# Kernel optimization log

Measured on AMD Instinct MI355X. Metric: run time of the kernel, lower is better.

Reference implementation:

```python
import jax, jax.numpy as jnp
import numpy as np

N = 100000      # total nodes (100 graphs x 1000 nodes each)
G = 100         # graphs per batch
F_IN = 12       # node_features (temporal window)
F_OUT = 32      # DCRNN hidden size (hardcoded in module)
K = 5           # diffusion (Chebyshev) steps (hardcoded)
C = 4           # num_classes
E = 16 * N      # edges: ring (N) + random (15N)


def setup_inputs() -> dict:
    key = jax.random.key(0)
    ks = jax.random.split(key, 12)
    x = jax.random.normal(ks[0], (N, F_IN), dtype=jnp.float32)
    ring = jnp.arange(N, dtype=jnp.int32)
    src = jnp.concatenate([ring, jax.random.randint(ks[1], (15 * N,), 0, N, dtype=jnp.int32)])
    dst = jnp.concatenate([(ring + 1) % N, jax.random.randint(ks[2], (15 * N,), 0, N, dtype=jnp.int32)])
    edge_index = jnp.stack([src, dst])  # [2, E]
    edge_weight = jax.random.uniform(ks[3], (E,), dtype=jnp.float32, minval=0.1, maxval=1.0)
    batch = (jnp.arange(N, dtype=jnp.int32) * G) // N  # sorted graph ids, 1000 nodes per graph
    s = 0.1
    return dict(
        x=x, edge_index=edge_index, edge_weight=edge_weight, batch=batch,
        W_z=jax.random.normal(ks[4], (2, K, F_IN + F_OUT, F_OUT), jnp.float32) * s,
        b_z=jax.random.normal(ks[5], (F_OUT,), jnp.float32) * s,
        W_r=jax.random.normal(ks[6], (2, K, F_IN + F_OUT, F_OUT), jnp.float32) * s,
        b_r=jax.random.normal(ks[7], (F_OUT,), jnp.float32) * s,
        W_h=jax.random.normal(ks[8], (2, K, F_IN + F_OUT, F_OUT), jnp.float32) * s,
        b_h=jax.random.normal(ks[9], (F_OUT,), jnp.float32) * s,
        W_lin=jax.random.normal(ks[10], (F_OUT, C), jnp.float32) * s,
        b_lin=jax.random.normal(ks[11], (C,), jnp.float32) * s,
    )


def reference(x, edge_index, edge_weight, batch, W_z, b_z, W_r, b_r, W_h, b_h, W_lin, b_lin):
    row, col = edge_index[0], edge_index[1]
    # weighted in/out degrees (to_dense_adj sums duplicate edges, same as segment_sum)
    deg_out_inv = 1.0 / jax.ops.segment_sum(edge_weight, row, num_segments=N)
    deg_in_inv = 1.0 / jax.ops.segment_sum(edge_weight, col, num_segments=N)
    norm_out = deg_out_inv[row][:, None]  # per-edge 1/deg_out(src)
    norm_in = deg_in_inv[row][:, None]    # per-edge 1/deg_in(src), as in DConv

    def prop_fwd(h):  # out[dst] += h[src]/deg_out[src]
        return jax.ops.segment_sum(norm_out * h[row], col, num_segments=N)

    def prop_rev(h):  # reverse (transposed) diffusion: out[src] += h[dst]/deg_in[src]
        return jax.ops.segment_sum(norm_in * h[col], row, num_segments=N)

    def dconv(Xc, W, b):
        # Chebyshev diffusion conv, W: [2, K, F_in+F_out, F_out]
        H = Xc @ (W[0, 0] + W[1, 0])
        T1o, T1i = prop_fwd(Xc), prop_rev(Xc)
        H = H + T1o @ W[0, 1] + T1i @ W[1, 1]
        T0o = T0i = Xc
        for k in range(2, K):
            T2o = 2.0 * prop_fwd(T1o) - T0o
            T2i = 2.0 * prop_rev(T1i) - T0i
            H = H + T2o @ W[0, k] + T2i @ W[1, k]
            T0o, T1o = T1o, T2o
            T0i, T1i = T1i, T2i
        return H + b

    # GRU gating with zero-initialized hidden state (H=None in module)
    Hst = jnp.zeros((N, F_OUT), x.dtype)
    XH = jnp.concatenate([x, Hst], axis=1)
    Z = jax.nn.sigmoid(dconv(XH, W_z, b_z))
    R = jax.nn.sigmoid(dconv(XH, W_r, b_r))
    XRH = jnp.concatenate([x, R * Hst], axis=1)
    H_tilde = jnp.tanh(dconv(XRH, W_h, b_h))
    H = Z * Hst + (1.0 - Z) * H_tilde

    h = jax.nn.relu(H) @ W_lin + b_lin            # [N, C]
    sums = jax.ops.segment_sum(h, batch, num_segments=G)
    counts = jax.ops.segment_sum(jnp.ones((N,), h.dtype), batch, num_segments=G)
    return sums / counts[:, None]                 # global_mean_pool -> [G, C]
```

## Files before the change

### kernel.cpp

```cpp
#include <hip/hip_runtime.h>
#include <math.h>

#define NN    100000
#define GG    100
#define FIN   12
#define FOUT  32
#define KD    5
#define CC    4
#define EE    1600000
#define ROWS  108
#define NBF   782
#define NBINS 1564
#define NBC   512
#define CHUNK 3125
#define TOTR  (2 * CHUNK)
#define NSEG  (NBINS * NBC)
#define SUBMAX 3072

__device__ __forceinline__ unsigned bfr(float f) {
    unsigned u = __float_as_uint(f);
    return (u + 0x7FFFu + ((u >> 16) & 1u)) >> 16;
}
__device__ __forceinline__ unsigned pack2(float a, float b) {
    return bfr(a) | (bfr(b) << 16);
}
#define BLO(u) __uint_as_float((u) << 16)
#define BHI(u) __uint_as_float((u) & 0xFFFF0000u)

__device__ __forceinline__ int chunk_of_block(int b) {
    return ((b & 7) << 6) | (b >> 3);
}


__global__ __launch_bounds__(512) void k_hist(const int* __restrict__ ei,
                                              int* __restrict__ hist_g) {
    __shared__ int hist[NBINS];
    for (int i = threadIdx.x; i < NBINS; i += 512) hist[i] = 0;
    __syncthreads();
    int chunk = chunk_of_block(blockIdx.x);
    int lo = chunk * CHUNK, hi = lo + CHUNK;
    for (int e = lo + threadIdx.x; e < hi; e += 512) {
        int s = ei[e], d = ei[EE + e];
        atomicAdd(&hist[d >> 7], 1);
        atomicAdd(&hist[NBF + (s >> 7)], 1);
    }
    __syncthreads();
    for (int i = threadIdx.x; i < NBINS; i += 512)
        hist_g[i * NBC + chunk] = hist[i];
}

__global__ __launch_bounds__(1024) void k_scan1(
        int* __restrict__ g, int* __restrict__ bsum,
        const float* __restrict__ Wz_in, const float* __restrict__ Wh_in,
        float* __restrict__ Wz, float* __restrict__ Wh,
        const float* __restrict__ b_lin, float* __restrict__ out,
        const float* __restrict__ x, uint2* __restrict__ xb) {
    __shared__ int sh[1024];
    int t = threadIdx.x;
    int i = blockIdx.x * 1024 + t;
    int v = g[i];
    sh[t] = v;
    __syncthreads();
    for (int d = 1; d < 1024; d <<= 1) {
        int x2 = sh[t];
        if (t >= d) x2 += sh[t - d];
        __syncthreads();
        sh[t] = x2;
        __syncthreads();
    }
    g[i] = sh[t] - v;
    if (t == 1023) bsum[blockIdx.x] = sh[1023];

    if (i < 2 * ROWS * FOUT) {
        int sel = i / (ROWS * FOUT);
        int rem = i - sel * ROWS * FOUT;
        int r = rem / FOUT;
        int f = rem - r * FOUT;
        int b = r / 12;
        int ii = r - b * 12;
        const float* Ws = sel ? Wh_in : Wz_in;
        float vv;
        if (b == 0)
            vv = Ws[(0 * KD + 0) * 44 * 32 + ii * 32 + f] + Ws[(1 * KD + 0) * 44 * 32 + ii * 32 + f];
        else if (b <= 4)
            vv = Ws[(0 * KD + b) * 44 * 32 + ii * 32 + f];
        else
            vv = Ws[(1 * KD + (b - 4)) * 44 * 32 + ii * 32 + f];
        (sel ? Wh : Wz)[r * FOUT + f] = vv;
    }
    int u = i - 2 * ROWS * FOUT;
    if (u >= 0 && u < GG * CC) out[u] = b_lin[u & 3];
    if (i < 3 * NN) {
        int n = i / 3, c = i - n * 3;
        float4 vf = *(const float4*)(x + (size_t)n * FIN + c * 4);
        xb[(size_t)n * 3 + c] = make_uint2(pack2(vf.x, vf.y), pack2(vf.z, vf.w));
    }
}

__global__ __launch_bounds__(1024) void k_scan3(int* __restrict__ g,
                                                const int* __restrict__ bsum,
                                                int* __restrict__ off,
                                                int* __restrict__ off_node) {
    __shared__ int sh[1024];
    int t = threadIdx.x;
    sh[t] = (t < blockIdx.x) ? bsum[t] : 0;
    __syncthreads();
    for (int d = 512; d > 0; d >>= 1) {
        if (t < d) sh[t] += sh[t + d];
        __syncthreads();
    }
    int base = sh[0];
    int i = blockIdx.x * 1024 + t;
    int v = g[i] + base;
    g[i] = v;
    if ((i & (NBC - 1)) == 0) off[i / NBC] = v;
    if (i == 0) { off[NBINS] = 2 * EE; off_node[2 * NN] = 2 * EE; }
}

__global__ __launch_bounds__(512) void k_place(const int* __restrict__ ei,
                                               const float* __restrict__ ew,
                                               const int* __restrict__ base_g,
                                               int2* __restrict__ recA) {
    __shared__ int2 ldsrec[TOTR];
    __shared__ int  lofs[NBINS];
    __shared__ int  cur[NBINS];
    __shared__ int  sbase[NBINS];
    __shared__ unsigned short binof[TOTR];
    int* psum = (int*)binof;
    int t = threadIdx.x;
    int chunk = chunk_of_block(blockIdx.x);

    for (int bin = t; bin < NBINS; bin += 512) {
        int b0 = base_g[bin * NBC + chunk];
        int b1;
        if (chunk < NBC - 1)      b1 = base_g[bin * NBC + chunk + 1];
        else if (bin < NBINS - 1) b1 = base_g[(bin + 1) * NBC];
        else                      b1 = 2 * EE;
        sbase[bin] = b0;
        lofs[bin] = b1 - b0;
        cur[bin] = 0;
    }
    __syncthreads();

    int i0 = t * 4;
    int v0 = 0, v1 = 0, v2 = 0, v3 = 0;
    if (i0 + 0 < NBINS) v0 = lofs[i0];
    if (i0 + 1 < NBINS) v1 = lofs[i0 + 1];
    if (i0 + 2 < NBINS) v2 = lofs[i0 + 2];
    if (i0 + 3 < NBINS) v3 = lofs[i0 + 3];
    int s = v0 + v1 + v2 + v3;
    psum[t] = s;
    __syncthreads();
    for (int d = 1; d < 512; d <<= 1) {
        int x = psum[t];
        if (t >= d) x += psum[t - d];
        __syncthreads();
        psum[t] = x;
        __syncthreads();
    }
    int run = psum[t] - s;
    __syncthreads();
    if (i0 + 0 < NBINS) { lofs[i0]     = run; run += v0; }
    if (i0 + 1 < NBINS) { lofs[i0 + 1] = run; run += v1; }
    if (i0 + 2 < NBINS) { lofs[i0 + 2] = run; run += v2; }
    if (i0 + 3 < NBINS) { lofs[i0 + 3] = run; run += v3; }
    __syncthreads();

    int lo = chunk * CHUNK;
    for (int e = lo + t; e < lo + CHUNK; e += 512) {
        int s2 = ei[e], d2 = ei[EE + e];
        float w = ew[e];
        int bf = d2 >> 7;
        int pf = lofs[bf] + atomicAdd(&cur[bf], 1);
        ldsrec[pf] = make_int2(s2 | ((d2 & 127) << 17), __float_as_int(w));
        binof[pf] = (unsigned short)bf;
        int br = NBF + (s2 >> 7);
        int pr = lofs[br] + atomicAdd(&cur[br], 1);
        ldsrec[pr] = make_int2(d2 | ((s2 & 127) << 17), __float_as_int(w));
        binof[pr] = (unsigned short)br;
    }
    __syncthreads();

    for (int i = t; i < TOTR; i += 512) {
        int b = binof[i];
        recA[sbase[b] + (i - lofs[b])] = ldsrec[i];
    }
}

__global__ __launch_bounds__(256) void k_subcsr(
        const int* __restrict__ off, const int2* __restrict__ recA,
        const float* __restrict__ x,
        int* __restrict__ off_node, int* __restrict__ rec2,
        float* __restrict__ dinv_in, float* __restrict__ dinv_out,
        uint2* __restrict__ gA) {
    __shared__ int2  seg[SUBMAX];
    __shared__ int   hist[128];
    __shared__ int   lofs[128];
    __shared__ int   cur[128];
    __shared__ float wsum[128];
    __shared__ float dl[128];
    int b = blockIdx.x;
    int t = threadIdx.x;
    if (t < 128) { hist[t] = 0; wsum[t] = 0.f; }
    __syncthreads();
    int e0 = off[b], e1 = off[b + 1];
    int cnt = e1 - e0;
    bool stg = (cnt <= SUBMAX);
    if (stg) {
        for (int i = t; i < cnt; i += 256) {
            int2 r = recA[e0 + i];
            seg[i] = r;
            int loc = r.x >> 17;
            atomicAdd(&hist[loc], 1);
            atomicAdd(&wsum[loc], __int_as_float(r.y));
        }
    } else {
        for (int i = t; i < cnt; i += 256) {
            int2 r = recA[e0 + i];
            int loc = r.x >> 17;
            atomicAdd(&hist[loc], 1);
            atomicAdd(&wsum[loc], __int_as_float(r.y));
        }
    }
    __syncthreads();
    if (t < 128) lofs[t] = hist[t];
    __syncthreads();
    for (int d = 1; d < 128; d <<= 1) {
        int v = 0;
        if (t < 128 && t >= d) v = lofs[t - d];
        __syncthreads();
        if (t < 128) lofs[t] += v;
        __syncthreads();
    }
    bool rev = b >= NBF;
    int base = (rev ? b - NBF : b) * 128;
    if (t < 128) {
        int ex = lofs[t] - hist[t];
        lofs[t] = ex;
        cur[t] = 0;
        int node = base + t;
        if (node < NN) {
            off_node[(rev ? NN : 0) + node] = e0 + ex;
            float inv = 1.f / wsum[t];
            dl[t] = inv;
            if (rev) dinv_out[node] = inv;
            else     dinv_in[node]  = inv;
        }
    }
    __syncthreads();
    if (stg) {
        for (int i = t; i < cnt; i += 256) {
            int rx = seg[i].x;
            int loc = rx >> 17;
            int pos = e0 + lofs[loc] + atomicAdd(&cur[loc], 1);
            rec2[pos] = rx & 0x1FFFF;
        }
    } else {
        for (int i = t; i < cnt; i += 256) {
            int rx = recA[e0 + i].x;
            int loc = rx >> 17;
            int pos = e0 + lofs[loc] + atomicAdd(&cur[loc], 1);
            rec2[pos] = rx & 0x1FFFF;
        }
    }
    if (rev) {
        __syncthreads();
        for (int i = t; i < 128 * 3; i += 256) {
            int loc = i / 3, cc = i - loc * 3;
            int node = base + loc;
            if (node < NN) {
                float4 v = *(const float4*)(x + (size_t)node * FIN + cc * 4);
                float sc = dl[loc];
                gA[(size_t)node * 3 + cc] =
                    make_uint2(pack2(v.x * sc, v.y * sc), pack2(v.z * sc, v.w * sc));
            }
        }
    }
}

#define LREC 2048
__global__ __launch_bounds__(256) void k_gather(
        const int* __restrict__ off_node, const int* __restrict__ rec2,
        const uint2* __restrict__ gIn, const uint2* __restrict__ hIn,
        const uint2* __restrict__ prevF, const uint2* __restrict__ prevR,
        const float* __restrict__ dinv_in, const float* __restrict__ dinv_out,
        uint2* __restrict__ outF, uint2* __restrict__ outR,
        uint2* __restrict__ gOut, float c) {
    __shared__ int lrec[LREC];
    int xcd = blockIdx.x & 7;
    int grp = blockIdx.x >> 3;
    bool rev = xcd >= 4;
    int dbase = rev ? NN : 0;
    int ub = (grp * 4 + (xcd & 3)) * 256;
    int lin = ub + threadIdx.x;

    int u1 = ub + 255; if (u1 > 3 * NN - 1) u1 = 3 * NN - 1;
    int node0 = ub / 3, node1 = u1 / 3;
    int w0 = off_node[dbase + node0];
    int w1 = off_node[dbase + node1 + 1];
    int wn = w1 - w0;
    bool useLds = (wn <= LREC);
    if (useLds) {
        for (int i = threadIdx.x; i < wn; i += 256) lrec[i] = rec2[w0 + i];
    }
    __syncthreads();

    if (lin < 3 * NN) {
        int node = lin / 3;
        int ch = lin - node * 3;
        int i0 = dbase + node;
        int e0 = off_node[i0], e1 = off_node[i0 + 1];
        const uint2* in = rev ? hIn : gIn;

        float ax = 0.f, ay = 0.f, az = 0.f, aw = 0.f;
        float bx = 0.f, by = 0.f, bz = 0.f, bw = 0.f;
        if (useLds) {
            int a0 = e0 - w0, a1 = e1 - w0;
            int e = a0;
            for (; e + 7 < a1; e += 8) {
                int n0 = lrec[e],     n1 = lrec[e + 1], n2 = lrec[e + 2], n3 = lrec[e + 3];
                int n4 = lrec[e + 4], n5 = lrec[e + 5], n6 = lrec[e + 6], n7 = lrec[e + 7];
                uint2 v0 = in[(size_t)n0 * 3 + ch];
                uint2 v1 = in[(size_t)n1 * 3 + ch];
                uint2 v2 = in[(size_t)n2 * 3 + ch];
                uint2 v3 = in[(size_t)n3 * 3 + ch];
                uint2 v4 = in[(size_t)n4 * 3 + ch];
                uint2 v5 = in[(size_t)n5 * 3 + ch];
                uint2 v6 = in[(size_t)n6 * 3 + ch];
                uint2 v7 = in[(size_t)n7 * 3 + ch];
                ax += BLO(v0.x); ay += BHI(v0.x); az += BLO(v0.y); aw += BHI(v0.y);
                bx += BLO(v1.x); by += BHI(v1.x); bz += BLO(v1.y); bw += BHI(v1.y);
                ax += BLO(v2.x); ay += BHI(v2.x); az += BLO(v2.y); aw += BHI(v2.y);
                bx += BLO(v3.x); by += BHI(v3.x); bz += BLO(v3.y); bw += BHI(v3.y);
                ax += BLO(v4.x); ay += BHI(v4.x); az += BLO(v4.y); aw += BHI(v4.y);
                bx += BLO(v5.x); by += BHI(v5.x); bz += BLO(v5.y); bw += BHI(v5.y);
                ax += BLO(v6.x); ay += BHI(v6.x); az += BLO(v6.y); aw += BHI(v6.y);
                bx += BLO(v7.x); by += BHI(v7.x); bz += BLO(v7.y); bw += BHI(v7.y);
            }
            for (; e < a1; ++e) {
                int n0 = lrec[e];
                uint2 v0 = in[(size_t)n0 * 3 + ch];
                ax += BLO(v0.x); ay += BHI(v0.x); az += BLO(v0.y); aw += BHI(v0.y);
            }
        } else {
            for (int e = e0; e < e1; ++e) {
                int n0 = rec2[e];
                uint2 v0 = in[(size_t)n0 * 3 + ch];
                ax += BLO(v0.x); ay += BHI(v0.x); az += BLO(v0.y); aw += BHI(v0.y);
            }
        }
        ax += bx; ay += by; az += bz; aw += bw;

        float sc = rev ? c * dinv_in[node] : c;
        ax *= sc; ay *= sc; az *= sc; aw *= sc;

        size_t o = (size_t)node * 3 + ch;
        if (prevF) {
            uint2 p = (rev ? prevR : prevF)[o];
            ax -= BLO(p.x); ay -= BHI(p.x); az -= BLO(p.y); aw -= BHI(p.y);
        }
        (rev ? outR : outF)[o] = make_uint2(pack2(ax, ay), pack2(az, aw));
        if (!rev && gOut) {
            float g = dinv_out[node];
            gOut[o] = make_uint2(pack2(g * ax, g * ay), pack2(g * az, g * aw));
        }
    }
}


__global__ __launch_bounds__(256) void k_fused(
        const float* __restrict__ x, const uint2* __restrict__ TS2,
        const float* __restrict__ Wz, const float* __restrict__ Wh,
        const float* __restrict__ bz, const float* __restrict__ bh,
        const float* __restrict__ Wlin, float* __restrict__ out) {
    __shared__ float rows[128][13];
    __shared__ float red[256 * CC];
    int g = blockIdx.x >> 3;
    int seg = blockIdx.x & 7;
    int base = g * 1000 + seg * 125;
    int tid = threadIdx.x;
    int lane = tid & 63;
    int wave = tid >> 6;
    int f0 = __builtin_amdgcn_readfirstlane(wave * 8);

    float az0[8], ah0[8], az1[8], ah1[8];
#pragma unroll
    for (int fi = 0; fi < 8; ++fi) {
        float vz = bz[f0 + fi], vh = bh[f0 + fi];
        az0[fi] = vz; ah0[fi] = vh; az1[fi] = vz; ah1[fi] = vh;
    }
    bool act1 = (lane + 64) < 125;

    for (int b = 0; b < 9; ++b) {
        __syncthreads();
        if (b == 0) {
            const float* src = x + (size_t)base * FIN;
            for (int q = tid; q < 375; q += 256) {
                float4 v = *(const float4*)(src + q * 4);
                int e = q * 4;
                int n0 = e / 12,       i0 = e - n0 * 12;       rows[n0][i0] = v.x;
                int n1 = (e + 1) / 12, i1 = (e + 1) - n1 * 12; rows[n1][i1] = v.y;
                int n2 = (e + 2) / 12, i2 = (e + 2) - n2 * 12; rows[n2][i2] = v.z;
                int n3 = (e + 3) / 12, i3 = (e + 3) - n3 * 12; rows[n3][i3] = v.w;
            }
        } else {
            const uint2* Tb = TS2 + (size_t)(b - 1) * NN * 3;
            for (int q = tid; q < 375; q += 256) {
                int n = q / 3, cc = q - n * 3;
                uint2 v = Tb[(size_t)(base + n) * 3 + cc];
                rows[n][cc * 4 + 0] = BLO(v.x);
                rows[n][cc * 4 + 1] = BHI(v.x);
                rows[n][cc * 4 + 2] = BLO(v.y);
                rows[n][cc * 4 + 3] = BHI(v.y);
            }
        }
        __syncthreads();
        const float* wzr = Wz + b * 12 * FOUT + f0;
        const float* whr = Wh + b * 12 * FOUT + f0;
#pragma unroll
        for (int i = 0; i < FIN; ++i) {
            float v0 = rows[lane][i];
            float v1 = rows[lane + 64][i];
#pragma unroll
            for (int fi = 0; fi < 8; ++fi) {
                float wz = wzr[i * FOUT + fi];
                float wh = whr[i * FOUT + fi];
                az0[fi] = fmaf(v0, wz, az0[fi]);
                az1[fi] = fmaf(v1, wz, az1[fi]);
                ah0[fi] = fmaf(v0, wh, ah0[fi]);
                ah1[fi] = fmaf(v1, wh, ah1[fi]);
            }
        }
    }

    float o[CC] = {0.f, 0.f, 0.f, 0.f};
#pragma unroll
    for (int fi = 0; fi < 8; ++fi) {
        float z = 1.f / (1.f + __expf(-az0[fi]));
        float e2 = __expf(2.f * ah0[fi]);
        float th = 1.f - 2.f / (e2 + 1.f);
        float hv = fmaxf((1.f - z) * th, 0.f);
#pragma unroll
        for (int c = 0; c < CC; ++c) o[c] = fmaf(hv, Wlin[(f0 + fi) * 4 + c], o[c]);
    }
    if (act1) {
#pragma unroll
        for (int fi = 0; fi < 8; ++fi) {
            float z = 1.f / (1.f + __expf(-az1[fi]));
            float e2 = __expf(2.f * ah1[fi]);
            float th = 1.f - 2.f / (e2 + 1.f);
            float hv = fmaxf((1.f - z) * th, 0.f);
#pragma unroll
            for (int c = 0; c < CC; ++c) o[c] = fmaf(hv, Wlin[(f0 + fi) * 4 + c], o[c]);
        }
    }

#pragma unroll
    for (int c = 0; c < CC; ++c) red[tid * CC + c] = o[c];
    __syncthreads();
    for (int st = 128; st > 0; st >>= 1) {
        if (tid < st) {
#pragma unroll
            for (int c = 0; c < CC; ++c) red[tid * CC + c] += red[(tid + st) * CC + c];
        }
        __syncthreads();
    }
    if (tid == 0) {
#pragma unroll
        for (int c = 0; c < CC; ++c) atomicAdd(out + g * CC + c, red[c] * 0.001f);
    }
}


extern "C" void kernel_launch(void* const* d_in, const int* in_sizes, int n_in,
                              void* d_out, int out_size, void* d_ws, size_t ws_size,
                              hipStream_t stream) {
    const float* x     = (const float*)d_in[0];
    const int*   ei    = (const int*)d_in[1];
    const float* ew    = (const float*)d_in[2];
    const float* W_z   = (const float*)d_in[4];
    const float* b_z   = (const float*)d_in[5];
    const float* W_h   = (const float*)d_in[8];
    const float* b_h   = (const float*)d_in[9];
    const float* W_lin = (const float*)d_in[10];
    const float* b_lin = (const float*)d_in[11];
    float* out = (float*)d_out;

    int*   rec2     = (int*)d_ws;
    unsigned* TSb   = (unsigned*)(rec2 + 2 * (size_t)EE);
    int2*  recA     = (int2*)TSb;
    int*   hist_g   = rec2;
    int*   bsumS    = rec2 + NSEG;
    unsigned* gAu   = TSb + (size_t)8 * NN * 6 + 1600000;
    unsigned* gBu   = gAu + (size_t)NN * 6;
    unsigned* xbu   = gBu + (size_t)NN * 6;
    float* dinv_in  = (float*)(xbu + (size_t)NN * 6);
    float* dinv_out = dinv_in + NN;
    float* Wz       = dinv_out + NN;
    float* Wh       = Wz + ROWS * FOUT;
    int*   off      = (int*)(Wh + ROWS * FOUT);
    int*   off_node = off + NBINS + 1;

    uint2* TS2 = (uint2*)TSb;
    uint2* T1o = TS2 + (size_t)0 * NN * 3;
    uint2* T2o = TS2 + (size_t)1 * NN * 3;
    uint2* T3o = TS2 + (size_t)2 * NN * 3;
    uint2* T4o = TS2 + (size_t)3 * NN * 3;
    uint2* T1i = TS2 + (size_t)4 * NN * 3;
    uint2* T2i = TS2 + (size_t)5 * NN * 3;
    uint2* T3i = TS2 + (size_t)6 * NN * 3;
    uint2* T4i = TS2 + (size_t)7 * NN * 3;
    uint2* gA = (uint2*)gAu;
    uint2* gB = (uint2*)gBu;
    uint2* xb = (uint2*)xbu;

    dim3 B(256);
    int nbG = 2344;
    int nbScan = NSEG / 1024;

    k_hist<<<NBC, 512, 0, stream>>>(ei, hist_g);
    k_scan1<<<nbScan, 1024, 0, stream>>>(hist_g, bsumS, W_z, W_h, Wz, Wh, b_lin, out, x, xb);
    k_scan3<<<nbScan, 1024, 0, stream>>>(hist_g, bsumS, off, off_node);
    k_place<<<NBC, 512, 0, stream>>>(ei, ew, hist_g, recA);
    k_subcsr<<<NBINS, B, 0, stream>>>(off, recA, x, off_node, rec2, dinv_in, dinv_out, gA);

    k_gather<<<nbG, B, 0, stream>>>(off_node, rec2, gA, xb,  nullptr, nullptr, dinv_in, dinv_out, T1o, T1i, gB, 1.f);
    k_gather<<<nbG, B, 0, stream>>>(off_node, rec2, gB, T1i, xb,      xb,      dinv_in, dinv_out, T2o, T2i, gA, 2.f);
    k_gather<<<nbG, B, 0, stream>>>(off_node, rec2, gA, T2i, T1o,     T1i,     dinv_in, dinv_out, T3o, T3i, gB, 2.f);
    k_gather<<<nbG, B, 0, stream>>>(off_node, rec2, gB, T3i, T2o,     T2i,     dinv_in, dinv_out, T4o, T4i, nullptr, 2.f);

    k_fused<<<8 * GG, B, 0, stream>>>(x, TS2, Wz, Wh, b_z, b_h, W_lin, out);
}
```

Measured before the change: 285.4 us.

## Fuse final diffusion gather step into the gating/pooling kernel

Removes the last k_gather launch and computes the T4 forward and reverse diffusion terms inside k_fused on demand, staging each block's edge indices in shared memory. This drops the T4o/T4i global writes and re-reads plus one kernel launch. In exchange, k_fused does irregular gathers with only 800 blocks, which may give lower occupancy and latency hiding than the standalone gather kernel with 2344 blocks. The extra shared-memory buffer may also reduce occupancy.

Result: no change. 283.6 us (-0.6%).

```diff
diff --git a/kernel.cpp b/kernel.cpp
--- a/kernel.cpp
+++ b/kernel.cpp
@@ -368,13 +368,17 @@
 }
 
 
+#define FREC 2560
 __global__ __launch_bounds__(256) void k_fused(
         const float* __restrict__ x, const uint2* __restrict__ TS2,
+        const int* __restrict__ off_node, const int* __restrict__ rec2,
+        const uint2* __restrict__ gB, const float* __restrict__ dinv_in,
         const float* __restrict__ Wz, const float* __restrict__ Wh,
         const float* __restrict__ bz, const float* __restrict__ bh,
         const float* __restrict__ Wlin, float* __restrict__ out) {
     __shared__ float rows[128][13];
     __shared__ float red[256 * CC];
+    __shared__ int   frec[FREC];
     int g = blockIdx.x >> 3;
     int seg = blockIdx.x & 7;
     int base = g * 1000 + seg * 125;
@@ -382,6 +386,10 @@
     int lane = tid & 63;
     int wave = tid >> 6;
     int f0 = __builtin_amdgcn_readfirstlane(wave * 8);
+
+    const uint2* T2o = TS2 + (size_t)1 * NN * 3;
+    const uint2* T2i = TS2 + (size_t)5 * NN * 3;
+    const uint2* T3i = TS2 + (size_t)6 * NN * 3;
 
     float az0[8], ah0[8], az1[8], ah1[8];
 #pragma unroll
@@ -402,6 +410,43 @@
                 int n1 = (e + 1) / 12, i1 = (e + 1) - n1 * 12; rows[n1][i1] = v.y;
                 int n2 = (e + 2) / 12, i2 = (e + 2) - n2 * 12; rows[n2][i2] = v.z;
                 int n3 = (e + 3) / 12, i3 = (e + 3) - n3 * 12; rows[n3][i3] = v.w;
+            }
+        } else if (b == 4 || b == 8) {
+            bool revd = (b == 8);
+            int dbase = revd ? NN : 0;
+            const uint2* gin  = revd ? T3i : gB;
+            const uint2* prev = revd ? T2i : T2o;
+            int w0 = off_node[dbase + base];
+            int w1 = off_node[dbase + base + 125];
+            int wn = w1 - w0;
+            bool useLds = (wn <= FREC);
+            if (useLds) {
+                for (int i = tid; i < wn; i += 256) frec[i] = rec2[w0 + i];
+            }
+            __syncthreads();
+            for (int q = tid; q < 375; q += 256) {
+                int n = q / 3, cc = q - n * 3;
+                int node = base + n;
+                int e0 = off_node[dbase + node], e1 = off_node[dbase + node + 1];
+                float ax = 0.f, ay = 0.f, az = 0.f, aw = 0.f;
+                if (useLds) {
+#pragma unroll 4
+                    for (int e = e0 - w0; e < e1 - w0; ++e) {
+                        uint2 v = gin[(size_t)frec[e] * 3 + cc];
+                        ax += BLO(v.x); ay += BHI(v.x); az += BLO(v.y); aw += BHI(v.y);
+                    }
+                } else {
+                    for (int e = e0; e < e1; ++e) {
+                        uint2 v = gin[(size_t)rec2[e] * 3 + cc];
+                        ax += BLO(v.x); ay += BHI(v.x); az += BLO(v.y); aw += BHI(v.y);
+                    }
+                }
+                float sc = revd ? 2.f * dinv_in[node] : 2.f;
+                uint2 p = prev[(size_t)node * 3 + cc];
+                rows[n][cc * 4 + 0] = ax * sc - BLO(p.x);
+                rows[n][cc * 4 + 1] = ay * sc - BHI(p.x);
+                rows[n][cc * 4 + 2] = az * sc - BLO(p.y);
+                rows[n][cc * 4 + 3] = aw * sc - BHI(p.y);
             }
         } else {
             const uint2* Tb = TS2 + (size_t)(b - 1) * NN * 3;
@@ -505,11 +550,9 @@
     uint2* T1o = TS2 + (size_t)0 * NN * 3;
     uint2* T2o = TS2 + (size_t)1 * NN * 3;
     uint2* T3o = TS2 + (size_t)2 * NN * 3;
-    uint2* T4o = TS2 + (size_t)3 * NN * 3;
     uint2* T1i = TS2 + (size_t)4 * NN * 3;
     uint2* T2i = TS2 + (size_t)5 * NN * 3;
     uint2* T3i = TS2 + (size_t)6 * NN * 3;
-    uint2* T4i = TS2 + (size_t)7 * NN * 3;
     uint2* gA = (uint2*)gAu;
     uint2* gB = (uint2*)gBu;
     uint2* xb = (uint2*)xbu;
@@ -527,7 +570,7 @@
     k_gather<<<nbG, B, 0, stream>>>(off_node, rec2, gA, xb,  nullptr, nullptr, dinv_in, dinv_out, T1o, T1i, gB, 1.f);
     k_gather<<<nbG, B, 0, stream>>>(off_node, rec2, gB, T1i, xb,      xb,      dinv_in, dinv_out, T2o, T2i, gA, 2.f);
     k_gather<<<nbG, B, 0, stream>>>(off_node, rec2, gA, T2i, T1o,     T1i,     dinv_in, dinv_out, T3o, T3i, gB, 2.f);
-    k_gather<<<nbG, B, 0, stream>>>(off_node, rec2, gB, T3i, T2o,     T2i,     dinv_in, dinv_out, T4o, T4i, nullptr, 2.f);
-
-    k_fused<<<8 * GG, B, 0, stream>>>(x, TS2, Wz, Wh, b_z, b_h, W_lin, out);
-}
+
+    k_fused<<<8 * GG, B, 0, stream>>>(x, TS2, off_node, rec2, gB, dinv_in,
+                                      Wz, Wh, b_z, b_h, W_lin, out);
+}
```
